# Kernel optimization log

Hardware: AMD Instinct MI355X
Metric: run time of the kernel (lower is better)

Reference implementation:

```python
import jax, jax.numpy as jnp
import numpy as np

MODEL_DIM = 1024
NUM_HEADS = 16
HEAD_DIM = MODEL_DIM // NUM_HEADS
EPS = 1e-12
CHUNK = 128  # chunk size for the linear-attention recurrence


def setup_inputs() -> dict:
    key = jax.random.key(0)
    kx, kq, kk, kv, ko = jax.random.split(key, 5)
    b, l = 4, 4096
    x = jax.random.normal(kx, (b, l, MODEL_DIM), dtype=jnp.float32)
    # nn.Linear weights, init std=0.02, no bias; torch Linear computes x @ W.T
    Wq = 0.02 * jax.random.normal(kq, (MODEL_DIM, MODEL_DIM), dtype=jnp.float32)
    Wk = 0.02 * jax.random.normal(kk, (MODEL_DIM, MODEL_DIM), dtype=jnp.float32)
    Wv = 0.02 * jax.random.normal(kv, (MODEL_DIM, MODEL_DIM), dtype=jnp.float32)
    Wo = 0.02 * jax.random.normal(ko, (MODEL_DIM, MODEL_DIM), dtype=jnp.float32)
    return {"x": x, "Wq": Wq, "Wk": Wk, "Wv": Wv, "Wo": Wo}


def _pos_elu(t):
    # feature_map = F.elu(x) + 1
    return jax.nn.elu(t) + 1.0


def _linear_attention(q, k, v):
    # q,k,v: (b,h,l,d) with feature map already applied.
    # Causal linear attention: out_t = (q_t . sum_{s<=t} k_s v_s^T) / (q_t . sum_{s<=t} k_s) + EPS
    # Chunked recurrence over the (d,d) KV state avoids the (b,h,l,d,d) cumsum.
    b, h, l, d = q.shape
    nc = l // CHUNK
    qc = jnp.moveaxis(q.reshape(b, h, nc, CHUNK, d), 2, 0)  # (nc,b,h,C,d)
    kc = jnp.moveaxis(k.reshape(b, h, nc, CHUNK, d), 2, 0)
    vc = jnp.moveaxis(v.reshape(b, h, nc, CHUNK, d), 2, 0)
    mask = jnp.tril(jnp.ones((CHUNK, CHUNK), dtype=q.dtype))  # causal within chunk

    def step(carry, inp):
        S, z = carry  # S:(b,h,d,d) running sum k v^T; z:(b,h,d) running sum k
        qb, kb, vb = inp  # (b,h,C,d)
        scores = jnp.einsum('bhcd,bhsd->bhcs', qb, kb) * mask  # (b,h,C,C)
        num = jnp.einsum('bhcd,bhde->bhce', qb, S) + jnp.einsum('bhcs,bhse->bhce', scores, vb)
        den = jnp.einsum('bhcd,bhd->bhc', qb, z) + scores.sum(-1)  # (b,h,C)
        out = num / den[..., None] + EPS  # NOTE: eps added after division, as in source
        S = S + jnp.einsum('bhsd,bhse->bhde', kb, vb)
        z = z + kb.sum(axis=2)
        return (S, z), out

    S0 = jnp.zeros((b, h, d, d), dtype=q.dtype)
    z0 = jnp.zeros((b, h, d), dtype=q.dtype)
    _, outs = jax.lax.scan(step, (S0, z0), (qc, kc, vc))  # (nc,b,h,C,d)
    # -> (b, l, h, d)
    return jnp.moveaxis(outs, 0, 1).transpose(0, 3, 1, 2, 4).reshape(b, h * 0 + l // l, 0, 0) if False else outs


def reference(x, Wq, Wk, Wv, Wo):
    b, l, D = x.shape
    h, d = NUM_HEADS, HEAD_DIM
    # projections (torch Linear: x @ W.T), split heads -> (b,h,l,d)
    q = (x @ Wq.T).reshape(b, l, h, d).transpose(0, 2, 1, 3)
    k = (x @ Wk.T).reshape(b, l, h, d).transpose(0, 2, 1, 3)
    v = (x @ Wv.T).reshape(b, l, h, d).transpose(0, 2, 1, 3)
    q = _pos_elu(q)
    k = _pos_elu(k)
    outs = _linear_attention(q, k, v)  # (nc,b,h,C,d)
    nc = l // CHUNK
    # (nc,b,h,C,d) -> (b,nc,C,h,d) -> (b,l,D)  (matches transpose(1,2).view in torch)
    attn = outs.transpose(1, 0, 3, 2, 4).reshape(b, l, D)
    return attn @ Wo.T
```

## Files before the change

kernel.cpp:

```cpp
#include <hip/hip_runtime.h>
#include <stdint.h>

typedef float f32x4 __attribute__((ext_vector_type(4)));
typedef __bf16 bf16x8 __attribute__((ext_vector_type(8)));
typedef unsigned short u16x8 __attribute__((ext_vector_type(8)));

#define DEV __device__ __forceinline__

DEV unsigned short f2bf(float f) {
  unsigned int u = __float_as_uint(f);
  unsigned int r = (u + 0x7FFFu + ((u >> 16) & 1u)) >> 16;
  return (unsigned short)r;
}
DEV float b2f(unsigned short h) { return __uint_as_float(((unsigned int)h) << 16); }

DEV void gload16(const void* g, void* l) {
  __builtin_amdgcn_global_load_lds((__attribute__((address_space(1))) void*)(g),
                                   (__attribute__((address_space(3))) void*)(l), 16, 0, 0);
}

__global__ void cast_all(const float* __restrict__ x, const float* __restrict__ Wq,
                         const float* __restrict__ Wk, const float* __restrict__ Wv,
                         const float* __restrict__ Wo, unsigned short* __restrict__ xbf,
                         unsigned short* __restrict__ wqkv, unsigned short* __restrict__ wo) {
  int i = blockIdx.x * 256 + threadIdx.x;
  const float* src;
  unsigned short* dst;
  int j;
  if (i < 2097152) {
    src = x; dst = xbf; j = i;
  } else {
    int k = i - 2097152;
    int sel = k >> 17; j = k & 131071;
    src = (sel == 0) ? Wq : (sel == 1) ? Wk : (sel == 2) ? Wv : Wo;
    dst = (sel < 3) ? (wqkv + (size_t)sel * 1048576) : wo;
  }
  const float4* p = (const float4*)src + (size_t)j * 2;
  float4 a = p[0], b = p[1];
  u16x8 o;
  o[0] = f2bf(a.x); o[1] = f2bf(a.y); o[2] = f2bf(a.z); o[3] = f2bf(a.w);
  o[4] = f2bf(b.x); o[5] = f2bf(b.y); o[6] = f2bf(b.z); o[7] = f2bf(b.w);
  ((u16x8*)dst)[j] = o;
}

template<int MODE>
__global__ __launch_bounds__(256, 2) void gemm_bt(
    const unsigned short* __restrict__ A, const unsigned short* __restrict__ Bw,
    void* __restrict__ out0, unsigned short* __restrict__ qp,
    unsigned short* __restrict__ kp, unsigned short* __restrict__ vp,
    int K, int N, int nTn)
{
  __shared__ unsigned short sA[128 * 64];
  __shared__ unsigned short sB[128 * 64];
  int t = threadIdx.x, w = t >> 6, lane = t & 63, fr = lane & 15, fq = lane >> 4;
  int bid = blockIdx.x;
  int bm = bid / nTn, bn = bid % nTn;
  int wm = w >> 1, wn = w & 1;

  f32x4 acc[4][4];
  f32x4 z4 = {0.f, 0.f, 0.f, 0.f};
#pragma unroll
  for (int mi = 0; mi < 4; ++mi)
#pragma unroll
    for (int ni = 0; ni < 4; ++ni) acc[mi][ni] = z4;

  for (int k0 = 0; k0 < K; k0 += 64) {
#pragma unroll
    for (int i = 0; i < 4; ++i) {
      int p = (i * 4 + w) * 64 + lane;
      int r = p >> 3;
      int c8 = (p & 7) ^ (r & 7);
      gload16(A + (size_t)(bm * 128 + r) * K + k0 + c8 * 8, &sA[(i * 4 + w) * 512]);
      gload16(Bw + (size_t)(bn * 128 + r) * K + k0 + c8 * 8, &sB[(i * 4 + w) * 512]);
    }
    __syncthreads();
#pragma unroll
    for (int ks = 0; ks < 2; ++ks) {
      bf16x8 af[4], bg[4];
#pragma unroll
      for (int mi = 0; mi < 4; ++mi) {
        int r = wm * 64 + mi * 16 + fr;
        int c8 = (ks * 4 + fq) ^ (r & 7);
        af[mi] = *(const bf16x8*)&sA[(r * 8 + c8) * 8];
      }
#pragma unroll
      for (int ni = 0; ni < 4; ++ni) {
        int r = wn * 64 + ni * 16 + fr;
        int c8 = (ks * 4 + fq) ^ (r & 7);
        bg[ni] = *(const bf16x8*)&sB[(r * 8 + c8) * 8];
      }
#pragma unroll
      for (int mi = 0; mi < 4; ++mi)
#pragma unroll
        for (int ni = 0; ni < 4; ++ni)
          acc[mi][ni] = __builtin_amdgcn_mfma_f32_16x16x32_bf16(af[mi], bg[ni], acc[mi][ni], 0, 0, 0);
    }
    __syncthreads();
  }

  if (MODE == 0) {
    float* O = (float*)out0;
#pragma unroll
    for (int mi = 0; mi < 4; ++mi)
#pragma unroll
      for (int ni = 0; ni < 4; ++ni)
#pragma unroll
        for (int j = 0; j < 4; ++j) {
          int m = bm * 128 + wm * 64 + mi * 16 + fq * 4 + j;
          int n = bn * 128 + wn * 64 + ni * 16 + fr;
          O[(size_t)m * N + n] = acc[mi][ni][j];
        }
  } else {
    int tsel = (bn * 128) >> 10;
    unsigned short* base = (tsel == 0) ? qp : ((tsel == 1) ? kp : vp);
#pragma unroll
    for (int mi = 0; mi < 4; ++mi)
#pragma unroll
      for (int ni = 0; ni < 4; ++ni)
#pragma unroll
        for (int j = 0; j < 4; ++j) {
          int m = bm * 128 + wm * 64 + mi * 16 + fq * 4 + j;
          int n = bn * 128 + wn * 64 + ni * 16 + fr;
          int col1 = n & 1023;
          int h = col1 >> 6, d = col1 & 63;
          int b = m >> 12, l = m & 4095;
          float v = acc[mi][ni][j];
          if (tsel < 2) v = (v > 0.f) ? (v + 1.f) : __expf(v);
          base[(((size_t)(b * 16 + h)) * 4096 + l) * 64 + d] = f2bf(v);
        }
  }
}

__global__ __launch_bounds__(256) void chunk_state(
    const unsigned short* __restrict__ kb, const unsigned short* __restrict__ vb,
    float* __restrict__ Sbuf, float* __restrict__ zbuf)
{
  __shared__ unsigned short kT[64 * 136];
  __shared__ unsigned short vT[64 * 136];
  int t = threadIdx.x, w = t >> 6, lane = t & 63, fr = lane & 15, fq = lane >> 4;
  int bh = blockIdx.x >> 5, c = blockIdx.x & 31;
  size_t base = ((size_t)bh * 4096 + (size_t)c * 128) * 64;

  int s = t >> 1, d0 = (t & 1) * 32;
  const unsigned short* kpp = kb + base + (size_t)s * 64 + d0;
  const unsigned short* vpp = vb + base + (size_t)s * 64 + d0;
#pragma unroll
  for (int i = 0; i < 4; ++i) {
    u16x8 kr = *(const u16x8*)(kpp + i * 8);
    u16x8 vr = *(const u16x8*)(vpp + i * 8);
#pragma unroll
    for (int j = 0; j < 8; ++j) {
      int d = d0 + i * 8 + j;
      kT[d * 136 + s] = kr[j];
      vT[d * 136 + s] = vr[j];
    }
  }
  __syncthreads();

  f32x4 acc[4];
  f32x4 z4 = {0.f, 0.f, 0.f, 0.f};
#pragma unroll
  for (int n = 0; n < 4; ++n) acc[n] = z4;
#pragma unroll
  for (int ks = 0; ks < 4; ++ks) {
    bf16x8 av = *(const bf16x8*)&vT[(w * 16 + fr) * 136 + ks * 32 + fq * 8];
#pragma unroll
    for (int n = 0; n < 4; ++n) {
      bf16x8 bk = *(const bf16x8*)&kT[(n * 16 + fr) * 136 + ks * 32 + fq * 8];
      acc[n] = __builtin_amdgcn_mfma_f32_16x16x32_bf16(av, bk, acc[n], 0, 0, 0);
    }
  }
  size_t ob = ((size_t)bh * 32 + c) * 4096;
#pragma unroll
  for (int n = 0; n < 4; ++n)
#pragma unroll
    for (int j = 0; j < 4; ++j) {
      int e = w * 16 + fq * 4 + j, dd = n * 16 + fr;
      Sbuf[ob + (size_t)e * 64 + dd] = acc[n][j];
    }
  if (t < 64) {
    float z = 0.f;
#pragma unroll
    for (int i = 0; i < 16; ++i) {
      u16x8 kr = *(const u16x8*)&kT[t * 136 + i * 8];
#pragma unroll
      for (int j = 0; j < 8; ++j) z += b2f(kr[j]);
    }
    zbuf[((size_t)bh * 32 + c) * 64 + t] = z;
  }
}

__global__ __launch_bounds__(256) void scan_all(
    const float* __restrict__ Sbuf, const float* __restrict__ zbuf,
    unsigned short* __restrict__ Spref, float* __restrict__ zpref)
{
  if (blockIdx.x < 1024) {
    int idx = blockIdx.x * 256 + threadIdx.x;
    int bh = idx >> 12, i = idx & 4095;
    size_t base = (size_t)bh * 32 * 4096 + i;
    float run = 0.f;
#pragma unroll
    for (int c = 0; c < 32; ++c) {
      float v = Sbuf[base + (size_t)c * 4096];
      Spref[base + (size_t)c * 4096] = f2bf(run);
      run += v;
    }
  } else {
    int idx = (blockIdx.x - 1024) * 256 + threadIdx.x;
    size_t base = (size_t)(idx >> 6) * 32 * 64 + (idx & 63);
    float run = 0.f;
#pragma unroll
    for (int c = 0; c < 32; ++c) {
      float v = zbuf[base + c * 64];
      zpref[base + c * 64] = run;
      run += v;
    }
  }
}

__global__ __launch_bounds__(256, 2) void chunk_out(
    const unsigned short* __restrict__ qb, const unsigned short* __restrict__ kb,
    const unsigned short* __restrict__ vb, const unsigned short* __restrict__ Spref,
    const float* __restrict__ zpref, unsigned short* __restrict__ attn)
{
  __shared__ unsigned short sk[128 * 64];
  __shared__ unsigned short svt[64 * 128];
  __shared__ unsigned short ss[128 * 128];
  __shared__ unsigned short sS[80 * 64];
  int t = threadIdx.x, w = t >> 6, lane = t & 63, fr = lane & 15, fq = lane >> 4;
  int bh = blockIdx.x >> 5, c = blockIdx.x & 31;
  size_t qkbase = ((size_t)bh * 4096 + (size_t)c * 128) * 64;
  size_t sbase = ((size_t)bh * 32 + c) * 4096;

  u16x8 vreg[4];
#pragma unroll
  for (int i = 0; i < 4; ++i)
    vreg[i] = *(const u16x8*)(vb + qkbase + (size_t)(t * 4 + i) * 8);

#pragma unroll
  for (int i = 0; i < 4; ++i) {
    int p = t * 4 + i, r = p >> 3, c8 = p & 7;
    *(u16x8*)&sk[(r * 8 + (c8 ^ (r & 7))) * 8] = *(const u16x8*)(kb + qkbase + (size_t)p * 8);
  }
#pragma unroll
  for (int i = 0; i < 2; ++i) {
    int p = t * 2 + i, e = p >> 3, c8 = p & 7;
    *(u16x8*)&sS[(e * 8 + (c8 ^ (e & 7))) * 8] = *(const u16x8*)(Spref + sbase + (size_t)p * 8);
  }
  if (t < 64) sS[64 * 64 + t] = f2bf(zpref[((size_t)bh * 32 + c) * 64 + t]);
  {
    unsigned int* zz = (unsigned int*)&sS[65 * 64];
    for (int i = t; i < 480; i += 256) zz[i] = 0u;
  }
#pragma unroll
  for (int i = 0; i < 4; ++i) {
    int p = t * 4 + i, s = p >> 3, e0g = (p & 7) * 8;
#pragma unroll
    for (int j = 0; j < 8; ++j) {
      int e = e0g + j;
      svt[(e * 16 + ((s >> 3) ^ (e & 15))) * 8 + (s & 7)] = vreg[i][j];
    }
  }

  int rowbase = w * 32;
  bf16x8 aq[2][2];
#pragma unroll
  for (int mi = 0; mi < 2; ++mi)
#pragma unroll
    for (int kt = 0; kt < 2; ++kt) {
      int r = rowbase + mi * 16 + fr;
      aq[mi][kt] = *(const bf16x8*)(qb + qkbase + (size_t)r * 64 + kt * 32 + fq * 8);
    }
  __syncthreads();

  f32x4 accsT[2][8];
  f32x4 z4 = {0.f, 0.f, 0.f, 0.f};
#pragma unroll
  for (int mi = 0; mi < 2; ++mi)
#pragma unroll
    for (int ni = 0; ni < 8; ++ni) accsT[mi][ni] = z4;

#pragma unroll
  for (int ni = 0; ni < 8; ++ni)
#pragma unroll
    for (int kt = 0; kt < 2; ++kt) {
      int r = ni * 16 + fr;
      int c8 = (kt * 4 + fq) ^ (r & 7);
      bf16x8 bk = *(const bf16x8*)&sk[(r * 8 + c8) * 8];
      accsT[0][ni] = __builtin_amdgcn_mfma_f32_16x16x32_bf16(bk, aq[0][kt], accsT[0][ni], 0, 0, 0);
      accsT[1][ni] = __builtin_amdgcn_mfma_f32_16x16x32_bf16(bk, aq[1][kt], accsT[1][ni], 0, 0, 0);
    }

  float rs[2];
#pragma unroll
  for (int mi = 0; mi < 2; ++mi) {
    int m16 = mi * 16 + fr;
    float sum = 0.f;
#pragma unroll
    for (int ni = 0; ni < 8; ++ni)
#pragma unroll
      for (int j = 0; j < 4; ++j) {
        int s = ni * 16 + fq * 4 + j - rowbase;
        float v = (s <= m16) ? accsT[mi][ni][j] : 0.f;
        accsT[mi][ni][j] = v;
        sum += v;
      }
    sum += __shfl_xor(sum, 16, 64);
    sum += __shfl_xor(sum, 32, 64);
    rs[mi] = sum;
  }

#pragma unroll
  for (int mi = 0; mi < 2; ++mi) {
    int m = rowbase + mi * 16 + fr;
#pragma unroll
    for (int ni = 0; ni < 8; ++ni)
#pragma unroll
      for (int p = 0; p < 2; ++p) {
        unsigned int pk = (unsigned int)f2bf(accsT[mi][ni][2 * p]) |
                          ((unsigned int)f2bf(accsT[mi][ni][2 * p + 1]) << 16);
        int chunk = (2 * ni + (fq >> 1)) ^ (m & 15);
        *(unsigned int*)&ss[m * 128 + chunk * 8 + (fq & 1) * 4 + 2 * p] = pk;
      }
  }
  __syncthreads();

  f32x4 acco[2][4];
  f32x4 accd[2];
#pragma unroll
  for (int mi = 0; mi < 2; ++mi) {
    accd[mi] = z4;
#pragma unroll
    for (int ni = 0; ni < 4; ++ni) acco[mi][ni] = z4;
  }
#pragma unroll
  for (int kt = 0; kt < 2; ++kt) {
#pragma unroll
    for (int ni = 0; ni < 4; ++ni) {
      int r = ni * 16 + fr;
      int c8 = (kt * 4 + fq) ^ (r & 7);
      bf16x8 bS = *(const bf16x8*)&sS[(r * 8 + c8) * 8];
      acco[0][ni] = __builtin_amdgcn_mfma_f32_16x16x32_bf16(aq[0][kt], bS, acco[0][ni], 0, 0, 0);
      acco[1][ni] = __builtin_amdgcn_mfma_f32_16x16x32_bf16(aq[1][kt], bS, acco[1][ni], 0, 0, 0);
    }
    {
      int r = 64 + fr;
      int c8 = (kt * 4 + fq) ^ (r & 7);
      bf16x8 bz = *(const bf16x8*)&sS[(r * 8 + c8) * 8];
      accd[0] = __builtin_amdgcn_mfma_f32_16x16x32_bf16(aq[0][kt], bz, accd[0], 0, 0, 0);
      accd[1] = __builtin_amdgcn_mfma_f32_16x16x32_bf16(aq[1][kt], bz, accd[1], 0, 0, 0);
    }
  }
#pragma unroll
  for (int kt = 0; kt < 4; ++kt) {
    bf16x8 am[2];
#pragma unroll
    for (int mi = 0; mi < 2; ++mi) {
      int r = rowbase + mi * 16 + fr;
      int c8 = (kt * 4 + fq) ^ (r & 15);
      am[mi] = *(const bf16x8*)&ss[(r * 16 + c8) * 8];
    }
#pragma unroll
    for (int ni = 0; ni < 4; ++ni) {
      int r = ni * 16 + fr;
      int c8 = (kt * 4 + fq) ^ (r & 15);
      bf16x8 bv = *(const bf16x8*)&svt[(r * 16 + c8) * 8];
      acco[0][ni] = __builtin_amdgcn_mfma_f32_16x16x32_bf16(am[0], bv, acco[0][ni], 0, 0, 0);
      acco[1][ni] = __builtin_amdgcn_mfma_f32_16x16x32_bf16(am[1], bv, acco[1][ni], 0, 0, 0);
    }
  }

  int b = bh >> 4, h = bh & 15;
#pragma unroll
  for (int mi = 0; mi < 2; ++mi)
#pragma unroll
    for (int j = 0; j < 4; ++j) {
      float rsj = __shfl(rs[mi], fq * 4 + j, 64);
      float den = __shfl(accd[mi][j], (lane & 48), 64) + rsj;
      float rden = 1.f / den;
      int m = rowbase + mi * 16 + fq * 4 + j;
      size_t rowoff = ((size_t)b * 4096 + (size_t)c * 128 + m) * 1024 + h * 64;
#pragma unroll
      for (int ni = 0; ni < 4; ++ni) {
        int e = ni * 16 + fr;
        float o = acco[mi][ni][j] * rden + 1e-12f;
        attn[rowoff + e] = f2bf(o);
      }
    }
}

extern "C" void kernel_launch(void* const* d_in, const int* in_sizes, int n_in,
                              void* d_out, int out_size, void* d_ws, size_t ws_size,
                              hipStream_t stream) {
  (void)in_sizes; (void)n_in; (void)out_size; (void)ws_size;
  const float* x = (const float*)d_in[0];
  const float* Wq = (const float*)d_in[1];
  const float* Wk = (const float*)d_in[2];
  const float* Wv = (const float*)d_in[3];
  const float* Wo = (const float*)d_in[4];
  char* ws = (char*)d_ws;
  unsigned short* xbf  = (unsigned short*)(ws + 0);
  unsigned short* wqkv = (unsigned short*)(ws + 33554432);
  unsigned short* wo   = (unsigned short*)(ws + 39845888);
  unsigned short* q    = (unsigned short*)(ws + 41943040);
  unsigned short* k    = (unsigned short*)(ws + 75497472);
  unsigned short* v    = (unsigned short*)(ws + 109051904);
  unsigned short* attn = (unsigned short*)(ws + 142606336);
  float* Sbuf          = (float*)(ws + 176160768);
  unsigned short* Spref= (unsigned short*)(ws + 209715200);
  float* zbuf          = (float*)(ws + 226492416);
  float* zpref         = (float*)(ws + 227016704);

  cast_all<<<10240, 256, 0, stream>>>(x, Wq, Wk, Wv, Wo, xbf, wqkv, wo);
  gemm_bt<1><<<3072, 256, 0, stream>>>(xbf, wqkv, nullptr, q, k, v, 1024, 3072, 24);
  chunk_state<<<2048, 256, 0, stream>>>(k, v, Sbuf, zbuf);
  scan_all<<<1040, 256, 0, stream>>>(Sbuf, zbuf, Spref, zpref);
  chunk_out<<<2048, 256, 0, stream>>>(q, k, v, Spref, zpref, attn);
  gemm_bt<0><<<1024, 256, 0, stream>>>(attn, wo, d_out, nullptr, nullptr, nullptr, 1024, 1024, 8);
}
```

Before: 241.4 us.

## Store per-chunk KV state in bf16 with in-place scan; stage q in LDS

```diff
diff --git a/kernel.cpp b/kernel.cpp
--- a/kernel.cpp
+++ b/kernel.cpp
@@ -133,7 +133,7 @@
 
 __global__ __launch_bounds__(256) void chunk_state(
     const unsigned short* __restrict__ kb, const unsigned short* __restrict__ vb,
-    float* __restrict__ Sbuf, float* __restrict__ zbuf)
+    unsigned short* __restrict__ Spref, float* __restrict__ zbuf)
 {
   __shared__ unsigned short kT[64 * 136];
   __shared__ unsigned short vT[64 * 136];
@@ -176,7 +176,7 @@
 #pragma unroll
     for (int j = 0; j < 4; ++j) {
       int e = w * 16 + fq * 4 + j, dd = n * 16 + fr;
-      Sbuf[ob + (size_t)e * 64 + dd] = acc[n][j];
+      Spref[ob + (size_t)e * 64 + dd] = f2bf(acc[n][j]);
     }
   if (t < 64) {
     float z = 0.f;
@@ -191,22 +191,26 @@
 }
 
 __global__ __launch_bounds__(256) void scan_all(
-    const float* __restrict__ Sbuf, const float* __restrict__ zbuf,
-    unsigned short* __restrict__ Spref, float* __restrict__ zpref)
+    unsigned short* __restrict__ Spref, const float* __restrict__ zbuf,
+    float* __restrict__ zpref)
 {
-  if (blockIdx.x < 1024) {
+  if (blockIdx.x < 512) {
     int idx = blockIdx.x * 256 + threadIdx.x;
-    int bh = idx >> 12, i = idx & 4095;
-    size_t base = (size_t)bh * 32 * 4096 + i;
-    float run = 0.f;
+    int bh = idx >> 11, i = idx & 2047;
+    unsigned int* p32 = (unsigned int*)Spref;
+    size_t base = (size_t)bh * 32 * 2048 + i;
+    float r0 = 0.f, r1 = 0.f;
 #pragma unroll
     for (int c = 0; c < 32; ++c) {
-      float v = Sbuf[base + (size_t)c * 4096];
-      Spref[base + (size_t)c * 4096] = f2bf(run);
-      run += v;
+      unsigned int v = p32[base + (size_t)c * 2048];
+      float v0 = b2f((unsigned short)(v & 0xFFFFu));
+      float v1 = b2f((unsigned short)(v >> 16));
+      p32[base + (size_t)c * 2048] =
+          (unsigned int)f2bf(r0) | ((unsigned int)f2bf(r1) << 16);
+      r0 += v0; r1 += v1;
     }
   } else {
-    int idx = (blockIdx.x - 1024) * 256 + threadIdx.x;
+    int idx = (blockIdx.x - 512) * 256 + threadIdx.x;
     size_t base = (size_t)(idx >> 6) * 32 * 64 + (idx & 63);
     float run = 0.f;
 #pragma unroll
@@ -223,8 +227,8 @@
     const unsigned short* __restrict__ vb, const unsigned short* __restrict__ Spref,
     const float* __restrict__ zpref, unsigned short* __restrict__ attn)
 {
-  __shared__ unsigned short sk[128 * 64];
-  __shared__ unsigned short svt[64 * 128];
+  __shared__ unsigned short sq[128 * 64];
+  __shared__ unsigned short skv[128 * 64];
   __shared__ unsigned short ss[128 * 128];
   __shared__ unsigned short sS[80 * 64];
   int t = threadIdx.x, w = t >> 6, lane = t & 63, fr = lane & 15, fq = lane >> 4;
@@ -240,7 +244,9 @@
 #pragma unroll
   for (int i = 0; i < 4; ++i) {
     int p = t * 4 + i, r = p >> 3, c8 = p & 7;
-    *(u16x8*)&sk[(r * 8 + (c8 ^ (r & 7))) * 8] = *(const u16x8*)(kb + qkbase + (size_t)p * 8);
+    int sw = (r * 8 + (c8 ^ (r & 7))) * 8;
+    *(u16x8*)&sq[sw] = *(const u16x8*)(qb + qkbase + (size_t)p * 8);
+    *(u16x8*)&skv[sw] = *(const u16x8*)(kb + qkbase + (size_t)p * 8);
   }
 #pragma unroll
   for (int i = 0; i < 2; ++i) {
@@ -252,15 +258,7 @@
     unsigned int* zz = (unsigned int*)&sS[65 * 64];
     for (int i = t; i < 480; i += 256) zz[i] = 0u;
   }
-#pragma unroll
-  for (int i = 0; i < 4; ++i) {
-    int p = t * 4 + i, s = p >> 3, e0g = (p & 7) * 8;
-#pragma unroll
-    for (int j = 0; j < 8; ++j) {
-      int e = e0g + j;
-      svt[(e * 16 + ((s >> 3) ^ (e & 15))) * 8 + (s & 7)] = vreg[i][j];
-    }
-  }
+  __syncthreads();
 
   int rowbase = w * 32;
   bf16x8 aq[2][2];
@@ -269,9 +267,9 @@
 #pragma unroll
     for (int kt = 0; kt < 2; ++kt) {
       int r = rowbase + mi * 16 + fr;
-      aq[mi][kt] = *(const bf16x8*)(qb + qkbase + (size_t)r * 64 + kt * 32 + fq * 8);
-    }
-  __syncthreads();
+      int c8 = (kt * 4 + fq) ^ (r & 7);
+      aq[mi][kt] = *(const bf16x8*)&sq[(r * 8 + c8) * 8];
+    }
 
   f32x4 accsT[2][8];
   f32x4 z4 = {0.f, 0.f, 0.f, 0.f};
@@ -286,7 +284,7 @@
     for (int kt = 0; kt < 2; ++kt) {
       int r = ni * 16 + fr;
       int c8 = (kt * 4 + fq) ^ (r & 7);
-      bf16x8 bk = *(const bf16x8*)&sk[(r * 8 + c8) * 8];
+      bf16x8 bk = *(const bf16x8*)&skv[(r * 8 + c8) * 8];
       accsT[0][ni] = __builtin_amdgcn_mfma_f32_16x16x32_bf16(bk, aq[0][kt], accsT[0][ni], 0, 0, 0);
       accsT[1][ni] = __builtin_amdgcn_mfma_f32_16x16x32_bf16(bk, aq[1][kt], accsT[1][ni], 0, 0, 0);
     }
@@ -309,7 +307,17 @@
     sum += __shfl_xor(sum, 32, 64);
     rs[mi] = sum;
   }
-
+  __syncthreads();
+
+#pragma unroll
+  for (int i = 0; i < 4; ++i) {
+    int p = t * 4 + i, s = p >> 3, e0g = (p & 7) * 8;
+#pragma unroll
+    for (int j = 0; j < 8; ++j) {
+      int e = e0g + j;
+      skv[(e * 16 + ((s >> 3) ^ (e & 15))) * 8 + (s & 7)] = vreg[i][j];
+    }
+  }
 #pragma unroll
   for (int mi = 0; mi < 2; ++mi) {
     int m = rowbase + mi * 16 + fr;
@@ -364,7 +372,7 @@
     for (int ni = 0; ni < 4; ++ni) {
       int r = ni * 16 + fr;
       int c8 = (kt * 4 + fq) ^ (r & 15);
-      bf16x8 bv = *(const bf16x8*)&svt[(r * 16 + c8) * 8];
+      bf16x8 bv = *(const bf16x8*)&skv[(r * 16 + c8) * 8];
       acco[0][ni] = __builtin_amdgcn_mfma_f32_16x16x32_bf16(am[0], bv, acco[0][ni], 0, 0, 0);
       acco[1][ni] = __builtin_amdgcn_mfma_f32_16x16x32_bf16(am[1], bv, acco[1][ni], 0, 0, 0);
     }
@@ -406,15 +414,14 @@
   unsigned short* k    = (unsigned short*)(ws + 75497472);
   unsigned short* v    = (unsigned short*)(ws + 109051904);
   unsigned short* attn = (unsigned short*)(ws + 142606336);
-  float* Sbuf          = (float*)(ws + 176160768);
-  unsigned short* Spref= (unsigned short*)(ws + 209715200);
-  float* zbuf          = (float*)(ws + 226492416);
-  float* zpref         = (float*)(ws + 227016704);
+  unsigned short* Spref= (unsigned short*)(ws + 176160768);
+  float* zbuf          = (float*)(ws + 192937984);
+  float* zpref         = (float*)(ws + 193462272);
 
   cast_all<<<10240, 256, 0, stream>>>(x, Wq, Wk, Wv, Wo, xbf, wqkv, wo);
   gemm_bt<1><<<3072, 256, 0, stream>>>(xbf, wqkv, nullptr, q, k, v, 1024, 3072, 24);
-  chunk_state<<<2048, 256, 0, stream>>>(k, v, Sbuf, zbuf);
-  scan_all<<<1040, 256, 0, stream>>>(Sbuf, zbuf, Spref, zpref);
+  chunk_state<<<2048, 256, 0, stream>>>(k, v, Spref, zbuf);
+  scan_all<<<528, 256, 0, stream>>>(Spref, zbuf, zpref);
   chunk_out<<<2048, 256, 0, stream>>>(q, k, v, Spref, zpref, attn);
   gemm_bt<0><<<1024, 256, 0, stream>>>(attn, wo, d_out, nullptr, nullptr, nullptr, 1024, 1024, 8);
 }
```

Result: faster. 227.8 us (-5.6%).
